# Performance work log

Hardware: AMD Instinct MI355X
Metric: run time of the kernel (lower is better)

The kernel has to match this reference:

```python
import jax, jax.numpy as jnp
import numpy as np

N_NODES = 100000
N_EDGES = 3200000
N_FEAT = 128
DIM = 256
N_CLASSES = 16
BN_EPS = 1e-5


def _glorot(key, shape):
    fan_in, fan_out = shape[0], shape[1]
    lim = float(np.sqrt(6.0 / (fan_in + fan_out)))
    return jax.random.uniform(key, shape, jnp.float32, -lim, lim)


def setup_inputs() -> dict:
    key = jax.random.key(0)
    ks = jax.random.split(key, 16)
    x = jax.random.normal(ks[0], (N_NODES, N_FEAT), jnp.float32)
    edge_index = jax.random.randint(ks[1], (2, N_EDGES), 0, N_NODES, jnp.int64)
    inp = {"x": x, "edge_index": edge_index}
    # conv1 MLP: num_features -> dim -> dim
    inp["w1a"] = _glorot(ks[2], (N_FEAT, DIM)); inp["b1a"] = jnp.zeros((DIM,), jnp.float32)
    inp["w1b"] = _glorot(ks[3], (DIM, DIM));    inp["b1b"] = jnp.zeros((DIM,), jnp.float32)
    inp["g1"] = jnp.ones((DIM,), jnp.float32);  inp["be1"] = jnp.zeros((DIM,), jnp.float32)
    # conv2 MLP
    inp["w2a"] = _glorot(ks[4], (DIM, DIM)); inp["b2a"] = jnp.zeros((DIM,), jnp.float32)
    inp["w2b"] = _glorot(ks[5], (DIM, DIM)); inp["b2b"] = jnp.zeros((DIM,), jnp.float32)
    inp["g2"] = jnp.ones((DIM,), jnp.float32); inp["be2"] = jnp.zeros((DIM,), jnp.float32)
    # conv3 MLP
    inp["w3a"] = _glorot(ks[6], (DIM, DIM)); inp["b3a"] = jnp.zeros((DIM,), jnp.float32)
    inp["w3b"] = _glorot(ks[7], (DIM, DIM)); inp["b3b"] = jnp.zeros((DIM,), jnp.float32)
    # fc2: dim -> num_classes
    inp["wfc"] = _glorot(ks[8], (DIM, N_CLASSES)); inp["bfc"] = jnp.zeros((N_CLASSES,), jnp.float32)
    return inp


def _gin_conv(h, src, dst, wa, ba, wb, bb):
    # sum-aggregate neighbor features: agg[i] = sum_{(j->i)} h[j]; eps=0 so root weight = 1
    agg = jax.ops.segment_sum(h[src], dst, num_segments=N_NODES)
    z = jax.nn.relu((h + agg) @ wa + ba)
    return z @ wb + bb


def _batchnorm(h, gamma, beta):
    # training-mode BN over node dim (biased variance, as torch forward)
    m = h.mean(axis=0)
    v = ((h - m) ** 2).mean(axis=0)
    return gamma * (h - m) / jnp.sqrt(v + BN_EPS) + beta


def reference(x, edge_index, w1a, b1a, w1b, b1b, g1, be1,
              w2a, b2a, w2b, b2b, g2, be2,
              w3a, b3a, w3b, b3b, wfc, bfc):
    src, dst = edge_index[0], edge_index[1]
    h = jax.nn.relu(_gin_conv(x, src, dst, w1a, b1a, w1b, b1b))
    h = _batchnorm(h, g1, be1)
    h = jax.nn.relu(_gin_conv(h, src, dst, w2a, b2a, w2b, b2b))
    h = _batchnorm(h, g2, be2)
    h = jax.nn.relu(_gin_conv(h, src, dst, w3a, b3a, w3b, b3b))
    # dropout p=0.5 is identity in eval mode
    logits = h @ wfc + bfc
    return jax.nn.log_softmax(logits, axis=-1)
```

## Files before the change

### kernel.cpp

```cpp
#include <hip/hip_runtime.h>

typedef unsigned int  u32;
typedef unsigned short u16;

#define NND 100000
#define MPAD 100096
#define NE  3200000
#define F0  128
#define DIM 256
#define NC  16

#define BSH   9
#define NBUCK 196
#define CAP   18432
#define EPB   8192

typedef __bf16 bf16x8 __attribute__((ext_vector_type(8)));
typedef float  f32x4  __attribute__((ext_vector_type(4)));

__device__ __forceinline__ float b2f(u16 h){ return __uint_as_float(((u32)h)<<16); }
__device__ __forceinline__ u16 f2b(float f){
    u32 u = __float_as_uint(f);
    return (u16)((u + 0x7fffu + ((u>>16)&1u)) >> 16);
}
__device__ __forceinline__ float lo16(u32 u){ return __uint_as_float(u<<16); }
__device__ __forceinline__ float hi16(u32 u){ return __uint_as_float(u & 0xffff0000u); }

__device__ __forceinline__ void gload16(const u16* g, u16* l){
    __builtin_amdgcn_global_load_lds(
        (const __attribute__((address_space(1))) u32*)g,
        (__attribute__((address_space(3))) u32*)l, 16, 0, 0);
}

__global__ void probe_kernel(const u32* __restrict__ xw, const int* __restrict__ ei,
                             int* __restrict__ mode, int* __restrict__ gcur,
                             float* __restrict__ stats){
    int t = threadIdx.x;
    if(t < NBUCK) gcur[t] = 0;
    #pragma unroll
    for(int i=0;i<4;i++) stats[t + 256*i] = 0.f;
    if(t==0){
        int insane = 0;
        for(int i=0;i<64;i++){
            u32 w  = xw[i];
            u32 lo = w & 0xffffu;
            u32 e  = (lo >> 7) & 0xff;
            if(lo != 0 && (e < 48 || e > 208)) insane++;
        }
        mode[0] = (insane > 8) ? 1 : 0;
        int zeros = 0;
        for(int i=0;i<16;i++) if(ei[2*i+1]==0) zeros++;
        mode[1] = (zeros==16) ? 1 : 0;
    }
}

__device__ __forceinline__ int ld_src(const int* ei, int i64f, long e){
    return i64f ? ei[2*e] : ei[e];
}
__device__ __forceinline__ int ld_dst(const int* ei, int i64f, long e){
    return i64f ? ei[2*((long)NE + e)] : ei[(long)NE + e];
}

__global__ __launch_bounds__(256) void bucketA(const int* __restrict__ ei,
        const int* __restrict__ mode, u32* __restrict__ bucketArr,
        int* __restrict__ gcur){
    __shared__ u32 stag[EPB];
    __shared__ u16 sbuck[EPB];
    __shared__ int cnt[NBUCK];
    __shared__ int ofs[NBUCK];
    __shared__ int wofs[NBUCK];
    __shared__ int gbase[NBUCK];
    __shared__ int ps[256];
    int tid = threadIdx.x;
    int i64f = mode[1];
    long e0 = (long)blockIdx.x * EPB;
    int n = (int)min((long)EPB, (long)NE - e0);
    if(tid < NBUCK) cnt[tid] = 0;
    __syncthreads();
    for(int i=tid;i<n;i+=256){
        int d = ld_dst(ei, i64f, e0+i);
        atomicAdd(&cnt[d>>BSH], 1);
    }
    __syncthreads();
    ps[tid] = (tid < NBUCK) ? cnt[tid] : 0;
    __syncthreads();
    for(int o=1;o<256;o<<=1){
        int v = (tid>=o) ? ps[tid-o] : 0;
        __syncthreads();
        ps[tid] += v;
        __syncthreads();
    }
    if(tid < NBUCK){
        int ex = ps[tid] - cnt[tid];
        ofs[tid] = ex; wofs[tid] = ex;
        gbase[tid] = cnt[tid] ? atomicAdd(&gcur[tid], cnt[tid]) : 0;
    }
    __syncthreads();
    for(int i=tid;i<n;i+=256){
        int s = ld_src(ei, i64f, e0+i);
        int d = ld_dst(ei, i64f, e0+i);
        int b = d>>BSH;
        int r = atomicAdd(&wofs[b], 1);
        stag[r]  = ((u32)s<<BSH) | (u32)(d & ((1<<BSH)-1));
        sbuck[r] = (u16)b;
    }
    __syncthreads();
    for(int i=tid;i<n;i+=256){
        int b = sbuck[i];
        int pos = gbase[b] + (i - ofs[b]);
        if(pos < CAP) bucketArr[(size_t)b*CAP + pos] = stag[i];
    }
}

__global__ __launch_bounds__(256) void bucketB(const u32* __restrict__ bucketArr,
        const int* __restrict__ gcnt,
        int* __restrict__ rp, int* __restrict__ ssrc){
    __shared__ u32 stag[CAP];
    __shared__ int deg[512];
    __shared__ int lrp[512];
    __shared__ int cur[512];
    __shared__ int ps[256];
    int b = blockIdx.x, tid = threadIdx.x;
    ps[tid] = (tid < NBUCK) ? gcnt[tid] : 0;
    __syncthreads();
    for(int o=1;o<256;o<<=1){
        int v = (tid>=o) ? ps[tid-o] : 0;
        __syncthreads();
        ps[tid] += v;
        __syncthreads();
    }
    int base = (b>0) ? ps[b-1] : 0;
    int n = min(gcnt[b], CAP);
    const u32* ba = bucketArr + (size_t)b*CAP;
    deg[tid] = 0; deg[tid+256] = 0;
    __syncthreads();
    for(int i=tid;i<n;i+=256){
        atomicAdd(&deg[ba[i] & 511], 1);
    }
    __syncthreads();
    ps[tid] = deg[2*tid] + deg[2*tid+1];
    __syncthreads();
    for(int o=1;o<256;o<<=1){
        int v = (tid>=o) ? ps[tid-o] : 0;
        __syncthreads();
        ps[tid] += v;
        __syncthreads();
    }
    {
        int ep = (tid==0) ? 0 : ps[tid-1];
        lrp[2*tid]   = ep;
        lrp[2*tid+1] = ep + deg[2*tid];
        cur[2*tid]   = lrp[2*tid];
        cur[2*tid+1] = lrp[2*tid+1];
    }
    __syncthreads();
    for(int i=tid;i<512;i+=256){
        int node = (b<<BSH) + i;
        if(node <= NND) rp[node] = base + lrp[i];
    }
    for(int i=tid;i<n;i+=256){
        u32 v = ba[i];
        int r = atomicAdd(&cur[v & 511], 1);
        stag[r] = v >> BSH;
    }
    __syncthreads();
    for(int i=tid;i<n;i+=256){
        ssrc[base + i] = (int)stag[i];
    }
}

__global__ void cvt_x(const float* __restrict__ xf, u16* __restrict__ Xc,
                      const int* __restrict__ mode){
    if(!mode[0]) return;
    size_t i = ((size_t)blockIdx.x*256 + threadIdx.x)*8;
    float4 a = *(const float4*)(xf+i);
    float4 b = *(const float4*)(xf+i+4);
    uint4 pk;
    pk.x = (u32)f2b(a.x) | ((u32)f2b(a.y)<<16);
    pk.y = (u32)f2b(a.z) | ((u32)f2b(a.w)<<16);
    pk.z = (u32)f2b(b.x) | ((u32)f2b(b.y)<<16);
    pk.w = (u32)f2b(b.z) | ((u32)f2b(b.w)<<16);
    *(uint4*)(Xc + i) = pk;
}

__device__ __forceinline__ float ldf(const void* p, int i, int f32f){
    return f32f ? ((const float*)p)[i] : b2f(((const u16*)p)[i]);
}
__global__ void merged_cvt(
        const void* w1a, const void* w1b, const void* w2a, const void* w2b,
        const void* w3a, const void* w3b, const void* wfc,
        const void* b1a, const void* b1b, const void* g1, const void* be1,
        const void* b2a, const void* b2b, const void* g2, const void* be2,
        const void* b3a, const void* b3b, const void* bfcp,
        u16* __restrict__ Wt1a, u16* __restrict__ Wt1b, u16* __restrict__ Wt2a,
        u16* __restrict__ Wt2b, u16* __restrict__ Wt3a, u16* __restrict__ Wt3b,
        u16* __restrict__ Wfc, u16* __restrict__ Vc, const int* __restrict__ mode){
    int b = blockIdx.x, t = threadIdx.x;
    int f32f = mode[0];
    if(b < 128){
        int id = b*256 + t;
        int k = id / DIM, n = id % DIM;
        Wt1a[n*F0 + k] = f2b(ldf(w1a, id, f32f));
        return;
    }
    b -= 128;
    if(b < 5*256){
        int wi = b >> 8;
        const void* W = (wi==0)?w1b:(wi==1)?w2a:(wi==2)?w2b:(wi==3)?w3a:w3b;
        u16* Wt = (wi==0)?Wt1b:(wi==1)?Wt2a:(wi==2)?Wt2b:(wi==3)?Wt3a:Wt3b;
        int id = (b & 255)*256 + t;
        int k = id / DIM, n = id % DIM;
        Wt[n*DIM + k] = f2b(ldf(W, id, f32f));
        return;
    }
    b -= 5*256;
    if(b < 16){
        int id = b*256 + t;
        int k = id / NC, c = id % NC;
        Wfc[c*DIM + k] = f2b(ldf(wfc, id, f32f));
        return;
    }
    b -= 16;
    {
        const void* ps[11] = {b1a,b1b,g1,be1,b2a,b2b,g2,be2,b3a,b3b,bfcp};
        int lens[11] = {DIM,DIM,DIM,DIM,DIM,DIM,DIM,DIM,DIM,DIM,NC};
        if(t < lens[b]) Vc[b*256 + t] = f2b(ldf(ps[b], t, f32f));
    }
}

template<int LPI>
__global__ __launch_bounds__(256) void agg2(const u16* __restrict__ hA,
        const u16* __restrict__ hB, const int* __restrict__ mode,
        const int* __restrict__ rp, const int* __restrict__ ssrc,
        u16* __restrict__ out,
        const float* __restrict__ stats, const u16* __restrict__ g,
        const u16* __restrict__ be, int use_bn, int M){
    const int F = LPI*8;
    const int IPW = 64/LPI;
    int node = blockIdx.x*4 + (threadIdx.x>>6);
    if(node >= M) return;
    int lane = threadIdx.x & 63;
    int li   = lane & (LPI-1);
    int slot = lane / LPI;
    const u16* h = (LPI==16 && mode[0]) ? hB : hA;
    const int boff = li*8;

    int e0 = rp[node], e1 = rp[node+1];
    int n_items = e1 - e0 + 1;
    float acc[8] = {0.f,0.f,0.f,0.f,0.f,0.f,0.f,0.f};

    auto item = [&](int i)->int { return (i==0) ? node : ssrc[e0 + i - 1]; };
    auto addu = [&](uint4 u){
        acc[0]+=lo16(u.x); acc[1]+=hi16(u.x);
        acc[2]+=lo16(u.y); acc[3]+=hi16(u.y);
        acc[4]+=lo16(u.z); acc[5]+=hi16(u.z);
        acc[6]+=lo16(u.w); acc[7]+=hi16(u.w);
    };

    int i = 0;
    for(; i + 8*IPW <= n_items; i += 8*IPW){
        int s[8];
        #pragma unroll
        for(int j=0;j<8;j++) s[j] = item(i + j*IPW + slot);
        uint4 u[8];
        #pragma unroll
        for(int j=0;j<8;j++) u[j] = *(const uint4*)(h + (size_t)s[j]*F + boff);
        #pragma unroll
        for(int j=0;j<8;j++) addu(u[j]);
    }
    for(; i + IPW <= n_items; i += IPW){
        int s = item(i + slot);
        addu(*(const uint4*)(h + (size_t)s*F + boff));
    }
    if(i < n_items){
        int r = n_items - i;
        if(slot < r){
            int s = item(i + slot);
            addu(*(const uint4*)(h + (size_t)s*F + boff));
        }
    }

    #pragma unroll
    for(int j=0;j<8;j++){
        if(LPI==16) acc[j] += __shfl_xor(acc[j], 16);
        acc[j] += __shfl_xor(acc[j], 32);
    }

    if(slot == 0){
        float res[8];
        if(use_bn){
            float inv_m = 1.0f / (float)M;
            float cnt = (float)n_items;
            #pragma unroll
            for(int j=0;j<8;j++){
                int f = boff + j;
                float mean = stats[f]*inv_m;
                float var  = fmaxf(stats[F+f]*inv_m - mean*mean, 0.f);
                float rstd = rsqrtf(var + 1e-5f);
                float gg = b2f(g[f]);
                float a = gg*rstd;
                float bb = b2f(be[f]) - a*mean;
                res[j] = a*acc[j] + cnt*bb;
            }
        } else {
            #pragma unroll
            for(int j=0;j<8;j++) res[j] = acc[j];
        }
        uint4 o;
        o.x = (u32)f2b(res[0]) | ((u32)f2b(res[1])<<16);
        o.y = (u32)f2b(res[2]) | ((u32)f2b(res[3])<<16);
        o.z = (u32)f2b(res[4]) | ((u32)f2b(res[5])<<16);
        o.w = (u32)f2b(res[6]) | ((u32)f2b(res[7])<<16);
        *(uint4*)(out + (size_t)node*F + boff) = o;
    }
}

#define FBM 64
#define FBK 32
#define ZP  264
__global__ __launch_bounds__(256) void mlp_fused(
        const u16* __restrict__ A, const u16* __restrict__ WaT,
        const u16* __restrict__ ba, const u16* __restrict__ WbT,
        const u16* __restrict__ bb, u16* __restrict__ C,
        int Ka, float* __restrict__ stats, int do_stats){
    __shared__ __align__(16) u16 lA[FBM*FBK];
    __shared__ __align__(16) u16 lB[DIM*FBK];
    __shared__ __align__(16) u16 zt[FBM*ZP];
    __shared__ float colS[DIM], colS2[DIM];
    int tid = threadIdx.x;
    int w = tid>>6, lane = tid&63;
    int q = lane>>4, mr = lane&15;
    int m0 = blockIdx.x*FBM;

    if(do_stats){ colS[tid]=0.f; colS2[tid]=0.f; }

    f32x4 acc[4][4];
    #pragma unroll
    for(int i=0;i<4;i++)
        #pragma unroll
        for(int c=0;c<4;c++) acc[i][c] = (f32x4){0.f,0.f,0.f,0.f};

    {
        const u16* gA = A + (size_t)(m0 + (tid>>2))*Ka + (tid&3)*8;
        u16* lAd = &lA[tid*16/2];
        for(int k0=0; k0<Ka; k0+=FBK){
            gload16(gA, lAd); gA += FBK;
            #pragma unroll
            for(int j=0;j<4;j++){
                int s = j*256 + tid;
                gload16(WaT + (size_t)(s>>2)*Ka + k0 + (s&3)*8, &lB[s*8]);
            }
            __syncthreads();
            bf16x8 af[4], bf[4];
            #pragma unroll
            for(int i=0;i<4;i++)
                af[i] = *reinterpret_cast<const bf16x8*>(&lA[(i*16+mr)*FBK + q*8]);
            #pragma unroll
            for(int c=0;c<4;c++)
                bf[c] = *reinterpret_cast<const bf16x8*>(&lB[(w*64+c*16+mr)*FBK + q*8]);
            #pragma unroll
            for(int i=0;i<4;i++)
                #pragma unroll
                for(int c=0;c<4;c++)
                    acc[i][c] = __builtin_amdgcn_mfma_f32_16x16x32_bf16(af[i], bf[c], acc[i][c], 0, 0, 0);
            __syncthreads();
        }
    }
    #pragma unroll
    for(int c=0;c<4;c++){
        int col = w*64 + c*16 + mr;
        float bav = b2f(ba[col]);
        #pragma unroll
        for(int i=0;i<4;i++){
            #pragma unroll
            for(int r=0;r<4;r++){
                int row = i*16 + q*4 + r;
                zt[row*ZP + col] = f2b(fmaxf(acc[i][c][r] + bav, 0.f));
            }
            acc[i][c] = (f32x4){0.f,0.f,0.f,0.f};
        }
    }
    __syncthreads();

    for(int k0=0; k0<DIM; k0+=FBK){
        #pragma unroll
        for(int j=0;j<4;j++){
            int s = j*256 + tid;
            gload16(WbT + (size_t)(s>>2)*DIM + k0 + (s&3)*8, &lB[s*8]);
        }
        __syncthreads();
        bf16x8 af[4], bf[4];
        #pragma unroll
        for(int i=0;i<4;i++)
            af[i] = *reinterpret_cast<const bf16x8*>(&zt[(i*16+mr)*ZP + k0 + q*8]);
        #pragma unroll
        for(int c=0;c<4;c++)
            bf[c] = *reinterpret_cast<const bf16x8*>(&lB[(w*64+c*16+mr)*FBK + q*8]);
        #pragma unroll
        for(int i=0;i<4;i++)
            #pragma unroll
            for(int c=0;c<4;c++)
                acc[i][c] = __builtin_amdgcn_mfma_f32_16x16x32_bf16(af[i], bf[c], acc[i][c], 0, 0, 0);
        __syncthreads();
    }

    #pragma unroll
    for(int c=0;c<4;c++){
        int col = w*64 + c*16 + mr;
        float bv = b2f(bb[col]);
        float s = 0.f, s2 = 0.f;
        #pragma unroll
        for(int i=0;i<4;i++){
            int row = m0 + i*16 + q*4;
            #pragma unroll
            for(int r=0;r<4;r++){
                float v = fmaxf(acc[i][c][r] + bv, 0.f);
                u16 o = f2b(v);
                C[(size_t)(row + r)*DIM + col] = o;
                if(do_stats && (row + r) < NND){
                    float vr = b2f(o);
                    s += vr; s2 += vr*vr;
                }
            }
        }
        if(do_stats){
            atomicAdd(&colS[col], s);
            atomicAdd(&colS2[col], s2);
        }
    }
    if(do_stats){
        __syncthreads();
        atomicAdd(&stats[tid], colS[tid]);
        atomicAdd(&stats[DIM+tid], colS2[tid]);
    }
}

__global__ __launch_bounds__(256) void fc_lsm(const u16* __restrict__ h,
        const u16* __restrict__ wfcT, const u16* __restrict__ bfc,
        void* __restrict__ out, const int* __restrict__ mode, int M){
    __shared__ float lds[256];
    __shared__ float rmx[16], rls[16];
    int tid = threadIdx.x;
    int r = tid>>4, c = tid&15;
    int row = blockIdx.x*16 + r;
    float acc = b2f(bfc[c]);
    const u16* hp = h + (size_t)row*DIM;
    const u16* wp = wfcT + c*DIM;
    for(int k=0;k<DIM;k+=8){
        uint4 hv = *(const uint4*)(hp+k);
        uint4 wv = *(const uint4*)(wp+k);
        acc += lo16(hv.x)*lo16(wv.x) + hi16(hv.x)*hi16(wv.x)
             + lo16(hv.y)*lo16(wv.y) + hi16(hv.y)*hi16(wv.y)
             + lo16(hv.z)*lo16(wv.z) + hi16(hv.z)*hi16(wv.z)
             + lo16(hv.w)*lo16(wv.w) + hi16(hv.w)*hi16(wv.w);
    }
    lds[tid] = acc;
    __syncthreads();
    if(c==0){
        float mx = -1e30f;
        for(int i=0;i<NC;i++) mx = fmaxf(mx, lds[r*NC+i]);
        float s = 0.f;
        for(int i=0;i<NC;i++) s += expf(lds[r*NC+i] - mx);
        rmx[r] = mx; rls[r] = logf(s);
    }
    __syncthreads();
    if(row < M){
        float v = acc - rmx[r] - rls[r];
        if(mode[0]) ((float*)out)[(size_t)row*NC + c] = v;
        else        ((u16*)out)[(size_t)row*NC + c] = f2b(v);
    }
}

extern "C" void kernel_launch(void* const* d_in, const int* in_sizes, int n_in,
                              void* d_out, int out_size, void* d_ws, size_t ws_size,
                              hipStream_t stream){
    const void* x   = d_in[0];
    const int*  ei  = (const int*)d_in[1];
    const void* w1a = d_in[2];  const void* b1a = d_in[3];
    const void* w1b = d_in[4];  const void* b1b = d_in[5];
    const void* g1  = d_in[6];  const void* be1 = d_in[7];
    const void* w2a = d_in[8];  const void* b2a = d_in[9];
    const void* w2b = d_in[10]; const void* b2b = d_in[11];
    const void* g2  = d_in[12]; const void* be2 = d_in[13];
    const void* w3a = d_in[14]; const void* b3a = d_in[15];
    const void* w3b = d_in[16]; const void* b3b = d_in[17];
    const void* wfc = d_in[18]; const void* bfc = d_in[19];

    char* base = (char*)d_ws;
    size_t off = 0;
    auto alloc = [&](size_t bytes)->void*{
        void* p = base + off;
        off = (off + bytes + 255) & ~(size_t)255;
        return p;
    };
    u16*  P     = (u16*)alloc((size_t)MPAD*DIM*2);
    u16*  Q     = (u16*)alloc((size_t)MPAD*DIM*2);
    int*  ssrc  = (int*)alloc((size_t)NE*4);
    u32*  bArr  = (u32*)alloc((size_t)NBUCK*CAP*4);
    int*  gcur  = (int*)alloc((size_t)NBUCK*4);
    int*  rp    = (int*)alloc((size_t)(NND+1)*4);
    float* stats= (float*)alloc(4*DIM*4);
    int*  mode  = (int*)alloc(16);
    u16* Wt1a = (u16*)alloc((size_t)F0*DIM*2);
    u16* Wt1b = (u16*)alloc((size_t)DIM*DIM*2);
    u16* Wt2a = (u16*)alloc((size_t)DIM*DIM*2);
    u16* Wt2b = (u16*)alloc((size_t)DIM*DIM*2);
    u16* Wt3a = (u16*)alloc((size_t)DIM*DIM*2);
    u16* Wt3b = (u16*)alloc((size_t)DIM*DIM*2);
    u16* Vc   = (u16*)alloc(11*256*2);
    u16* Wfc  = (u16*)alloc((size_t)DIM*NC*2);
    u16* Xc   = P;
    float* statsA = stats;
    float* statsB = stats + 2*DIM;

    probe_kernel<<<1, 256, 0, stream>>>((const u32*)x, ei, mode, gcur, stats);

    bucketA<<<(NE + EPB - 1)/EPB, 256, 0, stream>>>(ei, mode, bArr, gcur);
    bucketB<<<NBUCK, 256, 0, stream>>>(bArr, gcur, rp, ssrc);

    cvt_x<<<(NND*F0)/(256*8), 256, 0, stream>>>((const float*)x, Xc, mode);
    merged_cvt<<<128 + 5*256 + 16 + 11, 256, 0, stream>>>(
        w1a,w1b,w2a,w2b,w3a,w3b,wfc, b1a,b1b,g1,be1,b2a,b2b,g2,be2,b3a,b3b,bfc,
        Wt1a,Wt1b,Wt2a,Wt2b,Wt3a,Wt3b,Wfc,Vc, mode);

    int mgrid = MPAD/FBM;

    agg2<16><<<NND/4, 256, 0, stream>>>((const u16*)x, Xc, mode, rp, ssrc, Q,
                                        statsA, Vc, Vc, 0, NND);
    mlp_fused<<<mgrid, 256, 0, stream>>>(Q, Wt1a, Vc+0*256, Wt1b, Vc+1*256, P,
                                         F0, statsA, 1);

    agg2<32><<<NND/4, 256, 0, stream>>>(P, P, mode, rp, ssrc, Q,
                                        statsA, Vc+2*256, Vc+3*256, 1, NND);
    mlp_fused<<<mgrid, 256, 0, stream>>>(Q, Wt2a, Vc+4*256, Wt2b, Vc+5*256, P,
                                         DIM, statsB, 1);

    agg2<32><<<NND/4, 256, 0, stream>>>(P, P, mode, rp, ssrc, Q,
                                        statsB, Vc+6*256, Vc+7*256, 1, NND);
    mlp_fused<<<mgrid, 256, 0, stream>>>(Q, Wt3a, Vc+8*256, Wt3b, Vc+9*256, P,
                                         DIM, statsA, 0);

    fc_lsm<<<NND/16, 256, 0, stream>>>(P, Wfc, Vc+10*256, d_out, mode, NND);
}
```

Baseline: 1.110 ms.

## Fuse final FC and log-softmax into last MLP kernel; load GEMM operands directly

The standalone fc_lsm kernel is removed. The third mlp_fused launch now writes its ReLU output to LDS, runs a small MFMA matmul against the FC weights, and does the log-softmax with lane shuffles, so the final hidden layer never goes to global memory and is never read back. Separately, both GEMM stages drop LDS staging through global_load_lds and barriers, and read A and the weight tiles directly from global memory into registers. That removes barriers and LDS traffic, but each wave now fetches its own weight fragments from global/L2 with no sharing inside the block.

```diff
diff --git a/kernel.cpp b/kernel.cpp
--- a/kernel.cpp
+++ b/kernel.cpp
@@ -25,12 +25,6 @@
 }
 __device__ __forceinline__ float lo16(u32 u){ return __uint_as_float(u<<16); }
 __device__ __forceinline__ float hi16(u32 u){ return __uint_as_float(u & 0xffff0000u); }
-
-__device__ __forceinline__ void gload16(const u16* g, u16* l){
-    __builtin_amdgcn_global_load_lds(
-        (const __attribute__((address_space(1))) u32*)g,
-        (__attribute__((address_space(3))) u32*)l, 16, 0, 0);
-}
 
 __global__ void probe_kernel(const u32* __restrict__ xw, const int* __restrict__ ei,
                              int* __restrict__ mode, int* __restrict__ gcur,
@@ -316,15 +310,14 @@
 }
 
 #define FBM 64
-#define FBK 32
 #define ZP  264
 __global__ __launch_bounds__(256) void mlp_fused(
         const u16* __restrict__ A, const u16* __restrict__ WaT,
         const u16* __restrict__ ba, const u16* __restrict__ WbT,
         const u16* __restrict__ bb, u16* __restrict__ C,
-        int Ka, float* __restrict__ stats, int do_stats){
-    __shared__ __align__(16) u16 lA[FBM*FBK];
-    __shared__ __align__(16) u16 lB[DIM*FBK];
+        int Ka, float* __restrict__ stats, int do_stats,
+        int do_fc, const u16* __restrict__ WfcT, const u16* __restrict__ bfc,
+        void* __restrict__ out, const int* __restrict__ mode){
     __shared__ __align__(16) u16 zt[FBM*ZP];
     __shared__ float colS[DIM], colS2[DIM];
     int tid = threadIdx.x;
@@ -340,31 +333,19 @@
         #pragma unroll
         for(int c=0;c<4;c++) acc[i][c] = (f32x4){0.f,0.f,0.f,0.f};
 
-    {
-        const u16* gA = A + (size_t)(m0 + (tid>>2))*Ka + (tid&3)*8;
-        u16* lAd = &lA[tid*16/2];
-        for(int k0=0; k0<Ka; k0+=FBK){
-            gload16(gA, lAd); gA += FBK;
-            #pragma unroll
-            for(int j=0;j<4;j++){
-                int s = j*256 + tid;
-                gload16(WaT + (size_t)(s>>2)*Ka + k0 + (s&3)*8, &lB[s*8]);
-            }
-            __syncthreads();
-            bf16x8 af[4], bf[4];
-            #pragma unroll
-            for(int i=0;i<4;i++)
-                af[i] = *reinterpret_cast<const bf16x8*>(&lA[(i*16+mr)*FBK + q*8]);
+    for(int k0=0; k0<Ka; k0+=32){
+        bf16x8 af[4], bf[4];
+        #pragma unroll
+        for(int i=0;i<4;i++)
+            af[i] = *reinterpret_cast<const bf16x8*>(A + (size_t)(m0 + i*16 + mr)*Ka + k0 + q*8);
+        #pragma unroll
+        for(int c=0;c<4;c++)
+            bf[c] = *reinterpret_cast<const bf16x8*>(WaT + (size_t)(w*64 + c*16 + mr)*Ka + k0 + q*8);
+        #pragma unroll
+        for(int i=0;i<4;i++)
             #pragma unroll
             for(int c=0;c<4;c++)
-                bf[c] = *reinterpret_cast<const bf16x8*>(&lB[(w*64+c*16+mr)*FBK + q*8]);
-            #pragma unroll
-            for(int i=0;i<4;i++)
-                #pragma unroll
-                for(int c=0;c<4;c++)
-                    acc[i][c] = __builtin_amdgcn_mfma_f32_16x16x32_bf16(af[i], bf[c], acc[i][c], 0, 0, 0);
-            __syncthreads();
-        }
+                acc[i][c] = __builtin_amdgcn_mfma_f32_16x16x32_bf16(af[i], bf[c], acc[i][c], 0, 0, 0);
     }
     #pragma unroll
     for(int c=0;c<4;c++){
@@ -382,92 +363,89 @@
     }
     __syncthreads();
 
-    for(int k0=0; k0<DIM; k0+=FBK){
-        #pragma unroll
-        for(int j=0;j<4;j++){
-            int s = j*256 + tid;
-            gload16(WbT + (size_t)(s>>2)*DIM + k0 + (s&3)*8, &lB[s*8]);
-        }
-        __syncthreads();
+    for(int k0=0; k0<DIM; k0+=32){
         bf16x8 af[4], bf[4];
         #pragma unroll
         for(int i=0;i<4;i++)
             af[i] = *reinterpret_cast<const bf16x8*>(&zt[(i*16+mr)*ZP + k0 + q*8]);
         #pragma unroll
         for(int c=0;c<4;c++)
-            bf[c] = *reinterpret_cast<const bf16x8*>(&lB[(w*64+c*16+mr)*FBK + q*8]);
+            bf[c] = *reinterpret_cast<const bf16x8*>(WbT + (size_t)(w*64 + c*16 + mr)*DIM + k0 + q*8);
         #pragma unroll
         for(int i=0;i<4;i++)
             #pragma unroll
             for(int c=0;c<4;c++)
                 acc[i][c] = __builtin_amdgcn_mfma_f32_16x16x32_bf16(af[i], bf[c], acc[i][c], 0, 0, 0);
-        __syncthreads();
-    }
-
-    #pragma unroll
-    for(int c=0;c<4;c++){
-        int col = w*64 + c*16 + mr;
-        float bv = b2f(bb[col]);
-        float s = 0.f, s2 = 0.f;
-        #pragma unroll
-        for(int i=0;i<4;i++){
-            int row = m0 + i*16 + q*4;
-            #pragma unroll
-            for(int r=0;r<4;r++){
-                float v = fmaxf(acc[i][c][r] + bv, 0.f);
-                u16 o = f2b(v);
-                C[(size_t)(row + r)*DIM + col] = o;
-                if(do_stats && (row + r) < NND){
-                    float vr = b2f(o);
-                    s += vr; s2 += vr*vr;
+    }
+
+    if(!do_fc){
+        #pragma unroll
+        for(int c=0;c<4;c++){
+            int col = w*64 + c*16 + mr;
+            float bv = b2f(bb[col]);
+            float s = 0.f, s2 = 0.f;
+            #pragma unroll
+            for(int i=0;i<4;i++){
+                int row = m0 + i*16 + q*4;
+                #pragma unroll
+                for(int r=0;r<4;r++){
+                    float v = fmaxf(acc[i][c][r] + bv, 0.f);
+                    u16 o = f2b(v);
+                    C[(size_t)(row + r)*DIM + col] = o;
+                    if(do_stats && (row + r) < NND){
+                        float vr = b2f(o);
+                        s += vr; s2 += vr*vr;
+                    }
                 }
             }
+            if(do_stats){
+                atomicAdd(&colS[col], s);
+                atomicAdd(&colS2[col], s2);
+            }
         }
         if(do_stats){
-            atomicAdd(&colS[col], s);
-            atomicAdd(&colS2[col], s2);
-        }
-    }
-    if(do_stats){
-        __syncthreads();
-        atomicAdd(&stats[tid], colS[tid]);
-        atomicAdd(&stats[DIM+tid], colS2[tid]);
-    }
-}
-
-__global__ __launch_bounds__(256) void fc_lsm(const u16* __restrict__ h,
-        const u16* __restrict__ wfcT, const u16* __restrict__ bfc,
-        void* __restrict__ out, const int* __restrict__ mode, int M){
-    __shared__ float lds[256];
-    __shared__ float rmx[16], rls[16];
-    int tid = threadIdx.x;
-    int r = tid>>4, c = tid&15;
-    int row = blockIdx.x*16 + r;
-    float acc = b2f(bfc[c]);
-    const u16* hp = h + (size_t)row*DIM;
-    const u16* wp = wfcT + c*DIM;
-    for(int k=0;k<DIM;k+=8){
-        uint4 hv = *(const uint4*)(hp+k);
-        uint4 wv = *(const uint4*)(wp+k);
-        acc += lo16(hv.x)*lo16(wv.x) + hi16(hv.x)*hi16(wv.x)
-             + lo16(hv.y)*lo16(wv.y) + hi16(hv.y)*hi16(wv.y)
-             + lo16(hv.z)*lo16(wv.z) + hi16(hv.z)*hi16(wv.z)
-             + lo16(hv.w)*lo16(wv.w) + hi16(hv.w)*hi16(wv.w);
-    }
-    lds[tid] = acc;
-    __syncthreads();
-    if(c==0){
-        float mx = -1e30f;
-        for(int i=0;i<NC;i++) mx = fmaxf(mx, lds[r*NC+i]);
-        float s = 0.f;
-        for(int i=0;i<NC;i++) s += expf(lds[r*NC+i] - mx);
-        rmx[r] = mx; rls[r] = logf(s);
-    }
-    __syncthreads();
-    if(row < M){
-        float v = acc - rmx[r] - rls[r];
-        if(mode[0]) ((float*)out)[(size_t)row*NC + c] = v;
-        else        ((u16*)out)[(size_t)row*NC + c] = f2b(v);
+            __syncthreads();
+            atomicAdd(&stats[tid], colS[tid]);
+            atomicAdd(&stats[DIM+tid], colS2[tid]);
+        }
+    } else {
+        __syncthreads();
+        #pragma unroll
+        for(int c=0;c<4;c++){
+            int col = w*64 + c*16 + mr;
+            float bv = b2f(bb[col]);
+            #pragma unroll
+            for(int i=0;i<4;i++)
+                #pragma unroll
+                for(int r=0;r<4;r++)
+                    zt[(i*16 + q*4 + r)*ZP + col] = f2b(fmaxf(acc[i][c][r] + bv, 0.f));
+        }
+        __syncthreads();
+        f32x4 fa = (f32x4){0.f,0.f,0.f,0.f};
+        for(int k0=0; k0<DIM; k0+=32){
+            bf16x8 za = *reinterpret_cast<const bf16x8*>(&zt[(w*16+mr)*ZP + k0 + q*8]);
+            bf16x8 wb = *reinterpret_cast<const bf16x8*>(WfcT + (size_t)mr*DIM + k0 + q*8);
+            fa = __builtin_amdgcn_mfma_f32_16x16x32_bf16(za, wb, fa, 0, 0, 0);
+        }
+        float bv = b2f(bfc[mr]);
+        int f32o = mode[0];
+        #pragma unroll
+        for(int r=0;r<4;r++){
+            float val = fa[r] + bv;
+            float m = val;
+            #pragma unroll
+            for(int o=1;o<16;o<<=1) m = fmaxf(m, __shfl_xor(m, o));
+            float ex = expf(val - m);
+            float s = ex;
+            #pragma unroll
+            for(int o=1;o<16;o<<=1) s += __shfl_xor(s, o);
+            float res = val - m - logf(s);
+            int row = m0 + w*16 + q*4 + r;
+            if(row < NND){
+                if(f32o) ((float*)out)[(size_t)row*NC + mr] = res;
+                else     ((u16*)out)[(size_t)row*NC + mr] = f2b(res);
+            }
+        }
     }
 }
 
@@ -528,17 +506,15 @@
     agg2<16><<<NND/4, 256, 0, stream>>>((const u16*)x, Xc, mode, rp, ssrc, Q,
                                         statsA, Vc, Vc, 0, NND);
     mlp_fused<<<mgrid, 256, 0, stream>>>(Q, Wt1a, Vc+0*256, Wt1b, Vc+1*256, P,
-                                         F0, statsA, 1);
+                                         F0, statsA, 1, 0, Wfc, Vc+10*256, d_out, mode);
 
     agg2<32><<<NND/4, 256, 0, stream>>>(P, P, mode, rp, ssrc, Q,
                                         statsA, Vc+2*256, Vc+3*256, 1, NND);
     mlp_fused<<<mgrid, 256, 0, stream>>>(Q, Wt2a, Vc+4*256, Wt2b, Vc+5*256, P,
-                                         DIM, statsB, 1);
+                                         DIM, statsB, 1, 0, Wfc, Vc+10*256, d_out, mode);
 
     agg2<32><<<NND/4, 256, 0, stream>>>(P, P, mode, rp, ssrc, Q,
                                         statsB, Vc+6*256, Vc+7*256, 1, NND);
     mlp_fused<<<mgrid, 256, 0, stream>>>(Q, Wt3a, Vc+8*256, Wt3b, Vc+9*256, P,
-                                         DIM, statsA, 0);
-
-    fc_lsm<<<NND/16, 256, 0, stream>>>(P, Wfc, Vc+10*256, d_out, mode, NND);
-}
+                                         DIM, statsA, 0, 1, Wfc, Vc+10*256, d_out, mode);
+}
```

Measured after the change: 1.090 ms. Within noise of the previous version (-1.8%).
